# Kernel tuning notes

Hardware: AMD Instinct MI355X
Metric: run time of the kernel (lower is better)

## Reference

```python
import jax, jax.numpy as jnp
import numpy as np

D_MODEL = 1024
D_QKV = 64
N_HEADS = 16
SCALE = D_QKV ** 0.5


def setup_inputs() -> dict:
    key = jax.random.key(0)
    k1, k2, k3 = jax.random.split(key, 3)
    b, s = 2, 2048
    X = jax.random.normal(k1, (b, s, D_MODEL), dtype=jnp.float32)
    # torch Linear weight layout: [out_features, in_features]
    W_qkv = jax.random.normal(k2, (3 * D_QKV * N_HEADS, D_MODEL), dtype=jnp.float32) * (D_MODEL ** -0.5)
    W_out = jax.random.normal(k3, (D_MODEL, D_QKV * N_HEADS), dtype=jnp.float32) * ((D_QKV * N_HEADS) ** -0.5)
    mask = jnp.ones((b, s), dtype=bool)
    return {"X": X, "W_qkv": W_qkv, "W_out": W_out, "mask": mask}


def reference(X, W_qkv, W_out, mask):
    b, s, _ = X.shape
    # qkv projection, packed as (..., h, d_qkv, 3) per the original view/unbind
    qkv = (X @ W_qkv.T).reshape(b, s, N_HEADS, D_QKV, 3)
    q, k, v = qkv[..., 0], qkv[..., 1], qkv[..., 2]  # each [b, s, h, d]
    # scores: [b, h, s_q, s_k]
    scores = jnp.einsum('bshd,bthd->bhst', q, k) / SCALE
    scores = jnp.where(mask[:, None, None, :], scores, -jnp.inf)
    weights = jax.nn.softmax(scores, axis=-1)  # dropout p=0.0 -> identity
    attn_out = jnp.einsum('bhst,bthd->bshd', weights, v)  # [b, s, h, d]
    out = attn_out.reshape(b, s, N_HEADS * D_QKV) @ W_out.T
    return out
```

## Files before the change

### kernel.cpp

```cpp
#include <hip/hip_runtime.h>
#include <cstdint>
#include <cstdio>

typedef __attribute__((ext_vector_type(8))) short bf8;
typedef __attribute__((ext_vector_type(4))) float f4;
typedef __attribute__((ext_vector_type(4))) unsigned short us4;

__device__ __forceinline__ unsigned short f2bf(float f) {
  union { float f; unsigned int u; } v; v.f = f;
  unsigned int u = v.u;
  return (unsigned short)((u + 0x7FFFu + ((u >> 16) & 1u)) >> 16);
}

__device__ __forceinline__ unsigned int cvtpk(float a, float b) {
  unsigned int r;
  asm("v_cvt_pk_bf16_f32 %0, %1, %2" : "=v"(r) : "v"(a), "v"(b));
  return r;
}

__device__ __forceinline__ float ex2(float x) { return __builtin_amdgcn_exp2f(x); }

__device__ __forceinline__ void gload_lds16(const void* g, void* l) {
  __builtin_amdgcn_global_load_lds(
      (const __attribute__((address_space(1))) unsigned int*)g,
      (__attribute__((address_space(3))) unsigned int*)l, 16, 0, 0);
}

__device__ __forceinline__ f4 mfma16(bf8 a, bf8 b, f4 c) {
  return __builtin_amdgcn_mfma_f32_16x16x32_bf16(a, b, c, 0, 0, 0);
}

__global__ void k_cvt_all(const float* __restrict__ X, const float* __restrict__ Wqkv,
                          const float* __restrict__ Wout,
                          unsigned short* __restrict__ Xbf, unsigned short* __restrict__ Wperm,
                          unsigned short* __restrict__ WoutB) {
  const int nX = (2 * 2048 * 1024) / 4;
  const int nW = 3072 * 256;
  const int nO = (1024 * 1024) / 4;
  int i = blockIdx.x * blockDim.x + threadIdx.x;
  const int st = gridDim.x * blockDim.x;
  const int total = nX + nW + nO;
  for (; i < total; i += st) {
    if (i < nX) {
      float4 v = reinterpret_cast<const float4*>(X)[i];
      us4 o; o.x = f2bf(v.x); o.y = f2bf(v.y); o.z = f2bf(v.z); o.w = f2bf(v.w);
      reinterpret_cast<us4*>(Xbf)[i] = o;
    } else if (i < nX + nW) {
      const int ii = i - nX;
      const int np = ii >> 8, k4 = ii & 255;
      const int c = np >> 10, hd = np & 1023;
      const int h = hd >> 6, d = hd & 63;
      const int n = h * 192 + d * 3 + c;
      float4 v = reinterpret_cast<const float4*>(Wqkv + (size_t)n * 1024)[k4];
      us4 o; o.x = f2bf(v.x); o.y = f2bf(v.y); o.z = f2bf(v.z); o.w = f2bf(v.w);
      reinterpret_cast<us4*>(Wperm + (size_t)np * 1024)[k4] = o;
    } else {
      const int ii = i - nX - nW;
      float4 v = reinterpret_cast<const float4*>(Wout)[ii];
      us4 o; o.x = f2bf(v.x); o.y = f2bf(v.y); o.z = f2bf(v.z); o.w = f2bf(v.w);
      reinterpret_cast<us4*>(WoutB)[ii] = o;
    }
  }
}

__device__ __forceinline__ void gemm_stage(
    const unsigned short* __restrict__ A, const unsigned short* __restrict__ B,
    int K, int m0, int n0, int k0, char* As, char* Bs, int w, int srow_in, int sbo)
{
#pragma unroll
  for (int t = 0; t < 2; ++t) {
    const int c = w * 2 + t;
    const int r = c * 16 + srow_in;
    const int bo = sbo ^ ((r & 3) << 4);
    gload_lds16((const char*)A + ((size_t)(m0 + r) * K + k0) * 2 + bo, As + c * 1024);
    gload_lds16((const char*)B + ((size_t)(n0 + r) * K + k0) * 2 + bo, Bs + c * 1024);
  }
}

__device__ __forceinline__ void gemm_compute(
    const char* Asc, const char* Bsc, int wr, int wc, int lane, int kb, f4 (&acc)[4][4])
{
  bf8 af[4], bfr[4];
#pragma unroll
  for (int i = 0; i < 4; ++i) {
    const int R = wr + i * 16 + (lane & 15);
    af[i] = *(const bf8*)(Asc + R * 64 + (kb ^ ((R & 3) << 4)));
  }
#pragma unroll
  for (int j = 0; j < 4; ++j) {
    const int R = wc + j * 16 + (lane & 15);
    bfr[j] = *(const bf8*)(Bsc + R * 64 + (kb ^ ((R & 3) << 4)));
  }
#pragma unroll
  for (int i = 0; i < 4; ++i)
#pragma unroll
    for (int j = 0; j < 4; ++j)
      acc[i][j] = mfma16(af[i], bfr[j], acc[i][j]);
}

__device__ __forceinline__ void gemm_core(
    const unsigned short* __restrict__ A, const unsigned short* __restrict__ B,
    int K, int m0, int n0, char* As, char* Bs, f4 (&acc)[4][4])
{
  const int tid = threadIdx.x;
  const int lane = tid & 63;
  const int w = tid >> 6;
  const int wr = (w >> 1) << 6, wc = (w & 1) << 6;
  const int srow_in = lane >> 2;
  const int sbo = (lane & 3) << 4;
  const int kb = (lane >> 4) << 4;

  gemm_stage(A, B, K, m0, n0, 0, As, Bs, w, srow_in, sbo);
  __syncthreads();

  const int nk2 = K >> 6;
  for (int k2 = 0; k2 < nk2; ++k2) {
    const int k0 = k2 << 6;
    gemm_stage(A, B, K, m0, n0, k0 + 32, As + 8192, Bs + 8192, w, srow_in, sbo);
    gemm_compute(As, Bs, wr, wc, lane, kb, acc);
    __syncthreads();
    if (k2 + 1 < nk2)
      gemm_stage(A, B, K, m0, n0, k0 + 64, As, Bs, w, srow_in, sbo);
    gemm_compute(As + 8192, Bs + 8192, wr, wc, lane, kb, acc);
    __syncthreads();
  }
}

#define QSCALE 0.18033688011112042f

__global__ __launch_bounds__(256, 2)
void k_gemm_qkv(const unsigned short* __restrict__ A, const unsigned short* __restrict__ B,
                unsigned short* __restrict__ Qb, unsigned short* __restrict__ Kb,
                unsigned short* __restrict__ Vt)
{
  __shared__ unsigned short As[2][128 * 32];
  __shared__ unsigned short Bs[2][128 * 32];
  const int m0 = blockIdx.x * 128, n0 = blockIdx.y * 128;
  f4 acc[4][4] = {};
  gemm_core(A, B, 1024, m0, n0, (char*)As, (char*)Bs, acc);

  const int lane = threadIdx.x & 63, w = threadIdx.x >> 6;
  const int wr = (w >> 1) << 6, wc = (w & 1) << 6;
  const int region = n0 >> 10;
  if (region == 2) {
#pragma unroll
    for (int j = 0; j < 4; ++j) {
      const int n = n0 + wc + j * 16 + (lane & 15) - 2048;
#pragma unroll
      for (int i = 0; i < 4; ++i) {
        const int mb = m0 + wr + i * 16 + ((lane >> 4) << 2);
        uint2 pk;
        pk.x = cvtpk(acc[i][j][0], acc[i][j][1]);
        pk.y = cvtpk(acc[i][j][2], acc[i][j][3]);
        *(uint2*)&Vt[((size_t)((mb >> 11) * 1024 + n)) * 2048 + (mb & 2047)] = pk;
      }
    }
  } else {
#pragma unroll
    for (int j = 0; j < 4; ++j) {
      const int n = n0 + wc + j * 16 + (lane & 15);
#pragma unroll
      for (int i = 0; i < 4; ++i) {
        const int mb = m0 + wr + i * 16 + ((lane >> 4) << 2);
#pragma unroll
        for (int r = 0; r < 4; ++r) {
          const int m = mb + r;
          const float v = acc[i][j][r];
          if (region == 0) Qb[(size_t)m * 1024 + n] = f2bf(v * QSCALE);
          else             Kb[(size_t)m * 1024 + (n - 1024)] = f2bf(v);
        }
      }
    }
  }
}

__global__ __launch_bounds__(256, 2)
void k_gemm_out(const unsigned short* __restrict__ A, const unsigned short* __restrict__ B,
                float* __restrict__ O)
{
  __shared__ unsigned short As[2][128 * 32];
  __shared__ unsigned short Bs[2][128 * 32];
  const int m0 = blockIdx.x * 128, n0 = blockIdx.y * 128;
  f4 acc[4][4] = {};
  gemm_core(A, B, 1024, m0, n0, (char*)As, (char*)Bs, acc);

  const int lane = threadIdx.x & 63, w = threadIdx.x >> 6;
  const int wr = (w >> 1) << 6, wc = (w & 1) << 6;
#pragma unroll
  for (int j = 0; j < 4; ++j) {
    const int n = n0 + wc + j * 16 + (lane & 15);
#pragma unroll
    for (int i = 0; i < 4; ++i) {
      const int mb = m0 + wr + i * 16 + ((lane >> 4) << 2);
#pragma unroll
      for (int r = 0; r < 4; ++r)
        O[(size_t)(mb + r) * 1024 + n] = acc[i][j][r];
    }
  }
}

__global__ __launch_bounds__(512, 4)
void k_attn(const unsigned short* __restrict__ Qb, const unsigned short* __restrict__ Kb,
            const unsigned short* __restrict__ Vt, unsigned short* __restrict__ Ob)
{
  __shared__ unsigned short Ks[2][64 * 64];
  __shared__ unsigned short Vs[2][64 * 64];
  __shared__ unsigned short Ps[8][16 * 64];

  const int tid = threadIdx.x, lane = tid & 63, w = tid >> 6;
  const int lo = lane & 15, hi = lane >> 4;
  const int bh = blockIdx.y;
  const int b = bh >> 4, h = bh & 15;
  const int q0 = blockIdx.x * 128 + w * 16;
  const size_t base_qk = (size_t)b * 2048 * 1024 + h * 64;
  const size_t base_vt = ((size_t)b * 1024 + h * 64) * 2048;

  bf8 qf[2];
#pragma unroll
  for (int kk = 0; kk < 2; ++kk)
    qf[kk] = *(const bf8*)&Qb[base_qk + (size_t)(q0 + lo) * 1024 + kk * 32 + hi * 8];

  f4 oaccT[4] = {};
  float mrun = -1e30f, lrun = 0.f;

  const int srow = lane >> 3;
  const int sbo = (lane & 7) << 4;

  auto stage = [&](int t0s, int bufi) {
    const int r = w * 8 + srow;
    const int bo = sbo ^ ((r & 7) << 4);
    gload_lds16((const char*)Kb + (base_qk + (size_t)(t0s + r) * 1024) * 2 + bo,
                (char*)Ks + bufi * 8192 + w * 1024);
    gload_lds16((const char*)Vt + (base_vt + (size_t)r * 2048 + t0s) * 2 + bo,
                (char*)Vs + bufi * 8192 + w * 1024);
  };

  char* const prow = (char*)Ps[w] + lo * 128;
  const int swz = lo << 3;

  auto process = [&](const char* Kc, const char* Vc) {
    f4 s[4] = {};
#pragma unroll
    for (int kk = 0; kk < 2; ++kk) {
      bf8 kf[4];
#pragma unroll
      for (int j = 0; j < 4; ++j) {
        const int t = j * 16 + lo;
        kf[j] = *(const bf8*)(Kc + t * 128 + ((kk * 64 + hi * 16) ^ ((t & 7) << 4)));
      }
#pragma unroll
      for (int j = 0; j < 4; ++j)
        s[j] = mfma16(kf[j], qf[kk], s[j]);
    }

    float mx = fmaxf(fmaxf(s[0][0], s[0][1]), fmaxf(s[0][2], s[0][3]));
#pragma unroll
    for (int j = 1; j < 4; ++j)
      mx = fmaxf(mx, fmaxf(fmaxf(s[j][0], s[j][1]), fmaxf(s[j][2], s[j][3])));
    mx = fmaxf(mx, __shfl_xor(mx, 16));
    mx = fmaxf(mx, __shfl_xor(mx, 32));

    if (!__all(mx - mrun <= 8.0f)) {
      const float mnew = fmaxf(mrun, mx);
      const float al = ex2(mrun - mnew);
      lrun *= al;
#pragma unroll
      for (int jd = 0; jd < 4; ++jd)
#pragma unroll
        for (int r = 0; r < 4; ++r)
          oaccT[jd][r] *= al;
      mrun = mnew;
    }

    float rs = 0.f;
#pragma unroll
    for (int j = 0; j < 4; ++j) {
      const float p0 = ex2(s[j][0] - mrun), p1 = ex2(s[j][1] - mrun);
      const float p2 = ex2(s[j][2] - mrun), p3 = ex2(s[j][3] - mrun);
      rs += (p0 + p1) + (p2 + p3);
      uint2 pk; pk.x = cvtpk(p0, p1); pk.y = cvtpk(p2, p3);
      *(uint2*)(prow + ((j * 32 + hi * 8) ^ swz)) = pk;
    }
    rs += __shfl_xor(rs, 16);
    rs += __shfl_xor(rs, 32);
    lrun += rs;

#pragma unroll
    for (int kk = 0; kk < 2; ++kk) {
      bf8 vf[4];
#pragma unroll
      for (int jd = 0; jd < 4; ++jd) {
        const int dd = jd * 16 + lo;
        vf[jd] = *(const bf8*)(Vc + dd * 128 + ((kk * 64 + hi * 16) ^ ((dd & 7) << 4)));
      }
      uint2 ra = *(const uint2*)(prow + ((kk * 64 + hi * 16) ^ swz));
      uint2 rb = *(const uint2*)(prow + ((kk * 64 + hi * 16 + 8) ^ swz));
      union { unsigned int u[4]; bf8 v; } pu;
      pu.u[0] = ra.x; pu.u[1] = ra.y; pu.u[2] = rb.x; pu.u[3] = rb.y;
#pragma unroll
      for (int jd = 0; jd < 4; ++jd)
        oaccT[jd] = mfma16(vf[jd], pu.v, oaccT[jd]);
    }
  };

  stage(0, 0);
  __syncthreads();

  for (int it2 = 0; it2 < 16; ++it2) {
    const int t0 = it2 * 128;
    stage(t0 + 64, 1);
    process((const char*)Ks, (const char*)Vs);
    __syncthreads();
    if (it2 < 15) stage(t0 + 128, 0);
    process((const char*)Ks + 8192, (const char*)Vs + 8192);
    __syncthreads();
  }

  const float rl = 1.0f / lrun;
  const size_t rowb = base_qk + (size_t)(q0 + lo) * 1024;
#pragma unroll
  for (int jd = 0; jd < 4; ++jd) {
    uint2 o;
    o.x = cvtpk(oaccT[jd][0] * rl, oaccT[jd][1] * rl);
    o.y = cvtpk(oaccT[jd][2] * rl, oaccT[jd][3] * rl);
    *(uint2*)&Ob[rowb + jd * 16 + hi * 4] = o;
  }
}

extern "C" void kernel_launch(void* const* d_in, const int* in_sizes, int n_in,
                              void* d_out, int out_size, void* d_ws, size_t ws_size,
                              hipStream_t stream) {
  const float* X    = (const float*)d_in[0];
  const float* Wqkv = (const float*)d_in[1];
  const float* Wout = (const float*)d_in[2];
  float* out = (float*)d_out;

  char* ws = (char*)d_ws;
  unsigned short* Xbf   = (unsigned short*)(ws);
  unsigned short* Wperm = (unsigned short*)(ws + (8u  << 20));
  unsigned short* WoutB = (unsigned short*)(ws + (14u << 20));
  unsigned short* Qb    = (unsigned short*)(ws + (16u << 20));
  unsigned short* Kb    = (unsigned short*)(ws + (24u << 20));
  unsigned short* Vt    = (unsigned short*)(ws + (32u << 20));
  unsigned short* Ab    = (unsigned short*)(ws + (40u << 20));
  if (ws_size < (48u << 20)) {
    fprintf(stderr, "kernel_launch: ws_size %zu < 48MiB\n", ws_size);
  }

  k_cvt_all<<<2048, 256, 0, stream>>>(X, Wqkv, Wout, Xbf, Wperm, WoutB);
  k_gemm_qkv<<<dim3(32, 24), 256, 0, stream>>>(Xbf, Wperm, Qb, Kb, Vt);
  k_attn<<<dim3(16, 32), 512, 0, stream>>>(Qb, Kb, Vt, Ab);
  k_gemm_out<<<dim3(32, 8), 256, 0, stream>>>(Ab, WoutB, out);
}
```

Baseline: 191.1 us.

## Widen attention KV tiles to 128 and remap block indices for XCD locality

```diff
diff --git a/kernel.cpp b/kernel.cpp
--- a/kernel.cpp
+++ b/kernel.cpp
@@ -128,14 +128,16 @@
 
 #define QSCALE 0.18033688011112042f
 
-__global__ __launch_bounds__(256, 2)
+__global__ __launch_bounds__(256, 4)
 void k_gemm_qkv(const unsigned short* __restrict__ A, const unsigned short* __restrict__ B,
                 unsigned short* __restrict__ Qb, unsigned short* __restrict__ Kb,
                 unsigned short* __restrict__ Vt)
 {
   __shared__ unsigned short As[2][128 * 32];
   __shared__ unsigned short Bs[2][128 * 32];
-  const int m0 = blockIdx.x * 128, n0 = blockIdx.y * 128;
+  const int bid = blockIdx.x;
+  const int nid = (bid & 7) * 96 + (bid >> 3);
+  const int m0 = (nid & 31) * 128, n0 = (nid >> 5) * 128;
   f4 acc[4][4] = {};
   gemm_core(A, B, 1024, m0, n0, (char*)As, (char*)Bs, acc);
 
@@ -174,13 +176,15 @@
   }
 }
 
-__global__ __launch_bounds__(256, 2)
+__global__ __launch_bounds__(256, 4)
 void k_gemm_out(const unsigned short* __restrict__ A, const unsigned short* __restrict__ B,
                 float* __restrict__ O)
 {
   __shared__ unsigned short As[2][128 * 32];
   __shared__ unsigned short Bs[2][128 * 32];
-  const int m0 = blockIdx.x * 128, n0 = blockIdx.y * 128;
+  const int bid = blockIdx.x;
+  const int nid = (bid & 7) * 32 + (bid >> 3);
+  const int m0 = (nid & 31) * 128, n0 = (nid >> 5) * 128;
   f4 acc[4][4] = {};
   gemm_core(A, B, 1024, m0, n0, (char*)As, (char*)Bs, acc);
 
@@ -203,15 +207,17 @@
 void k_attn(const unsigned short* __restrict__ Qb, const unsigned short* __restrict__ Kb,
             const unsigned short* __restrict__ Vt, unsigned short* __restrict__ Ob)
 {
-  __shared__ unsigned short Ks[2][64 * 64];
-  __shared__ unsigned short Vs[2][64 * 64];
+  __shared__ unsigned short Ks[2][128 * 64];
+  __shared__ unsigned short Vs[2][64 * 128];
   __shared__ unsigned short Ps[8][16 * 64];
 
   const int tid = threadIdx.x, lane = tid & 63, w = tid >> 6;
   const int lo = lane & 15, hi = lane >> 4;
-  const int bh = blockIdx.y;
+  const int bid = blockIdx.y * 16 + blockIdx.x;
+  const int nid = (bid & 7) * 64 + (bid >> 3);
+  const int qt = nid & 15, bh = nid >> 4;
   const int b = bh >> 4, h = bh & 15;
-  const int q0 = blockIdx.x * 128 + w * 16;
+  const int q0 = qt * 128 + w * 16;
   const size_t base_qk = (size_t)b * 2048 * 1024 + h * 64;
   const size_t base_vt = ((size_t)b * 1024 + h * 64) * 2048;
 
@@ -223,39 +229,44 @@
   f4 oaccT[4] = {};
   float mrun = -1e30f, lrun = 0.f;
 
-  const int srow = lane >> 3;
-  const int sbo = (lane & 7) << 4;
-
-  auto stage = [&](int t0s, int bufi) {
-    const int r = w * 8 + srow;
-    const int bo = sbo ^ ((r & 7) << 4);
-    gload_lds16((const char*)Kb + (base_qk + (size_t)(t0s + r) * 1024) * 2 + bo,
-                (char*)Ks + bufi * 8192 + w * 1024);
-    gload_lds16((const char*)Vt + (base_vt + (size_t)r * 2048 + t0s) * 2 + bo,
-                (char*)Vs + bufi * 8192 + w * 1024);
+  const int sboK = (((lane & 7) ^ (lane >> 3)) << 4);
+
+  auto stage = [&](int t0s, char* Kd, char* Vd) {
+#pragma unroll
+    for (int t = 0; t < 2; ++t) {
+      const int c = w * 2 + t;
+      const int r = c * 8 + (lane >> 3);
+      gload_lds16((const char*)Kb + (base_qk + (size_t)(t0s + r) * 1024) * 2 + sboK,
+                  Kd + c * 1024);
+    }
+#pragma unroll
+    for (int t = 0; t < 2; ++t) {
+      const int c = w * 2 + t;
+      const int d = c * 4 + hi;
+      const int sv = ((lane & 15) ^ (d & 15)) << 4;
+      gload_lds16((const char*)Vt + (base_vt + (size_t)d * 2048 + t0s) * 2 + sv,
+                  Vd + c * 1024);
+    }
   };
 
   char* const prow = (char*)Ps[w] + lo * 128;
   const int swz = lo << 3;
 
   auto process = [&](const char* Kc, const char* Vc) {
-    f4 s[4] = {};
+    f4 s[8] = {};
 #pragma unroll
     for (int kk = 0; kk < 2; ++kk) {
-      bf8 kf[4];
-#pragma unroll
-      for (int j = 0; j < 4; ++j) {
+#pragma unroll
+      for (int j = 0; j < 8; ++j) {
         const int t = j * 16 + lo;
-        kf[j] = *(const bf8*)(Kc + t * 128 + ((kk * 64 + hi * 16) ^ ((t & 7) << 4)));
-      }
-#pragma unroll
-      for (int j = 0; j < 4; ++j)
-        s[j] = mfma16(kf[j], qf[kk], s[j]);
+        bf8 kf = *(const bf8*)(Kc + t * 128 + ((kk * 64 + hi * 16) ^ ((t & 7) << 4)));
+        s[j] = mfma16(kf, qf[kk], s[j]);
+      }
     }
 
     float mx = fmaxf(fmaxf(s[0][0], s[0][1]), fmaxf(s[0][2], s[0][3]));
 #pragma unroll
-    for (int j = 1; j < 4; ++j)
+    for (int j = 1; j < 8; ++j)
       mx = fmaxf(mx, fmaxf(fmaxf(s[j][0], s[j][1]), fmaxf(s[j][2], s[j][3])));
     mx = fmaxf(mx, __shfl_xor(mx, 16));
     mx = fmaxf(mx, __shfl_xor(mx, 32));
@@ -274,45 +285,52 @@
 
     float rs = 0.f;
 #pragma unroll
-    for (int j = 0; j < 4; ++j) {
-      const float p0 = ex2(s[j][0] - mrun), p1 = ex2(s[j][1] - mrun);
-      const float p2 = ex2(s[j][2] - mrun), p3 = ex2(s[j][3] - mrun);
-      rs += (p0 + p1) + (p2 + p3);
-      uint2 pk; pk.x = cvtpk(p0, p1); pk.y = cvtpk(p2, p3);
-      *(uint2*)(prow + ((j * 32 + hi * 8) ^ swz)) = pk;
+    for (int hh = 0; hh < 2; ++hh) {
+#pragma unroll
+      for (int j2 = 0; j2 < 4; ++j2) {
+        const f4 sv = s[hh * 4 + j2];
+        const float p0 = ex2(sv[0] - mrun), p1 = ex2(sv[1] - mrun);
+        const float p2 = ex2(sv[2] - mrun), p3 = ex2(sv[3] - mrun);
+        rs += (p0 + p1) + (p2 + p3);
+        uint2 pk; pk.x = cvtpk(p0, p1); pk.y = cvtpk(p2, p3);
+        *(uint2*)(prow + ((j2 * 32 + hi * 8) ^ swz)) = pk;
+      }
+#pragma unroll
+      for (int kkl = 0; kkl < 2; ++kkl) {
+        const int kkg = hh * 2 + kkl;
+        bf8 vf[4];
+#pragma unroll
+        for (int jd = 0; jd < 4; ++jd) {
+          const int dd = jd * 16 + lo;
+          vf[jd] = *(const bf8*)(Vc + dd * 256 + ((kkg * 64 + hi * 16) ^ ((dd & 15) << 4)));
+        }
+        uint2 ra = *(const uint2*)(prow + ((kkl * 64 + hi * 16) ^ swz));
+        uint2 rb = *(const uint2*)(prow + ((kkl * 64 + hi * 16 + 8) ^ swz));
+        union { unsigned int u[4]; bf8 v; } pu;
+        pu.u[0] = ra.x; pu.u[1] = ra.y; pu.u[2] = rb.x; pu.u[3] = rb.y;
+#pragma unroll
+        for (int jd = 0; jd < 4; ++jd)
+          oaccT[jd] = mfma16(vf[jd], pu.v, oaccT[jd]);
+      }
     }
     rs += __shfl_xor(rs, 16);
     rs += __shfl_xor(rs, 32);
     lrun += rs;
-
-#pragma unroll
-    for (int kk = 0; kk < 2; ++kk) {
-      bf8 vf[4];
-#pragma unroll
-      for (int jd = 0; jd < 4; ++jd) {
-        const int dd = jd * 16 + lo;
-        vf[jd] = *(const bf8*)(Vc + dd * 128 + ((kk * 64 + hi * 16) ^ ((dd & 7) << 4)));
-      }
-      uint2 ra = *(const uint2*)(prow + ((kk * 64 + hi * 16) ^ swz));
-      uint2 rb = *(const uint2*)(prow + ((kk * 64 + hi * 16 + 8) ^ swz));
-      union { unsigned int u[4]; bf8 v; } pu;
-      pu.u[0] = ra.x; pu.u[1] = ra.y; pu.u[2] = rb.x; pu.u[3] = rb.y;
-#pragma unroll
-      for (int jd = 0; jd < 4; ++jd)
-        oaccT[jd] = mfma16(vf[jd], pu.v, oaccT[jd]);
-    }
   };
 
-  stage(0, 0);
+  char* const K0 = (char*)Ks, *const K1 = (char*)Ks + 16384;
+  char* const V0 = (char*)Vs, *const V1 = (char*)Vs + 16384;
+
+  stage(0, K0, V0);
   __syncthreads();
 
-  for (int it2 = 0; it2 < 16; ++it2) {
-    const int t0 = it2 * 128;
-    stage(t0 + 64, 1);
-    process((const char*)Ks, (const char*)Vs);
+  for (int it2 = 0; it2 < 8; ++it2) {
+    const int t0 = it2 * 256;
+    stage(t0 + 128, K1, V1);
+    process(K0, V0);
     __syncthreads();
-    if (it2 < 15) stage(t0 + 128, 0);
-    process((const char*)Ks + 8192, (const char*)Vs + 8192);
+    if (it2 < 7) stage(t0 + 256, K0, V0);
+    process(K1, V1);
     __syncthreads();
   }
 
@@ -348,7 +366,7 @@
   }
 
   k_cvt_all<<<2048, 256, 0, stream>>>(X, Wqkv, Wout, Xbf, Wperm, WoutB);
-  k_gemm_qkv<<<dim3(32, 24), 256, 0, stream>>>(Xbf, Wperm, Qb, Kb, Vt);
+  k_gemm_qkv<<<768, 256, 0, stream>>>(Xbf, Wperm, Qb, Kb, Vt);
   k_attn<<<dim3(16, 32), 512, 0, stream>>>(Qb, Kb, Vt, Ab);
-  k_gemm_out<<<dim3(32, 8), 256, 0, stream>>>(Ab, WoutB, out);
-}
+  k_gemm_out<<<256, 256, 0, stream>>>(Ab, WoutB, out);
+}
```

Measured after the change: 194.2 us. Within noise of the previous version (+1.6%).
